# Performance work log

Measured on AMD Instinct MI355X. Metric: run time of the kernel, lower is better.

Reference implementation:

```python
import jax, jax.numpy as jnp
import numpy as np

B, NQ, NK = 1, 2048, 2048
A_DIM = M_DIM = 1024
H, KD, VD = 16, 64, 64


def setup_inputs() -> dict:
    key = jax.random.key(0)
    ks = jax.random.split(key, 8)
    return {
        "q_data": jax.random.normal(ks[0], (B, NQ, A_DIM), jnp.float32),
        "m_data": jax.random.normal(ks[1], (B, NK, M_DIM), jnp.float32),
        "batched_bias": jax.random.normal(ks[2], (B, H, NQ, NK), jnp.float32),
        "query_w": jax.random.normal(ks[3], (A_DIM, H, KD), jnp.float32) * 0.02,
        "query_b": jax.random.normal(ks[4], (1, H, KD), jnp.float32) * 0.02,
        "key_w": jax.random.normal(ks[5], (M_DIM, H, KD), jnp.float32) * 0.02,
        "value_w": jax.random.normal(ks[6], (M_DIM, H, VD), jnp.float32) * 0.02,
        "gating_w": jax.random.normal(ks[7], (A_DIM, H, VD), jnp.float32) * 0.02,
    }


def reference(q_data, m_data, batched_bias, query_w, query_b, key_w, value_w, gating_w):
    key_dim = query_w.shape[-1]
    scale = key_dim ** -0.5
    # fused: QKV projections + query bias + pair bias + softmax + gating
    q = (jnp.einsum('bqa,ahc->bqhc', q_data, query_w) + query_b) * scale  # [B,Q,H,KD]
    k = jnp.einsum('bka,ahc->bkhc', m_data, key_w)                        # [B,K,H,KD]
    v = jnp.einsum('bka,ahc->bkhc', m_data, value_w)                      # [B,K,H,VD]
    logits = jnp.einsum('bqhc,bkhc->bhqk', q, k) + batched_bias           # [B,H,Q,K]
    weights = jax.nn.softmax(logits, axis=-1)
    weighted = jnp.einsum('bhqk,bkhc->bqhc', weights, v)                  # [B,Q,H,VD]
    gate = jax.nn.sigmoid(jnp.einsum('bqa,ahc->bqhc', q_data, gating_w))  # [B,Q,H,VD]
    return gate * weighted
```

## Files before the change

kernel.cpp:

```cpp
#include <hip/hip_runtime.h>
#include <hip/hip_bf16.h>

typedef __bf16 bf16x8 __attribute__((ext_vector_type(8)));
typedef __bf16 bf16x4 __attribute__((ext_vector_type(4)));
typedef float  f32x4  __attribute__((ext_vector_type(4)));

typedef const __attribute__((address_space(1))) void* gptr_t;
typedef __attribute__((address_space(3))) void*       lptr_t;

#define NQ 2048
#define NK 2048
#define AD 1024
#define NH 16
#define HD 64
#define HC 1024

__global__ __launch_bounds__(256) void prep_convert(
    const float* __restrict__ q_data, const float* __restrict__ m_data,
    __bf16* __restrict__ aq, __bf16* __restrict__ am) {
  const int NEL4 = NQ * AD / 4;
  int gid = blockIdx.x * 256 + threadIdx.x;
  float4 v;
  __bf16* dst;
  if (gid < NEL4) { v = ((const float4*)q_data)[gid]; dst = aq + (size_t)gid * 4; }
  else            { v = ((const float4*)m_data)[gid - NEL4]; dst = am + (size_t)(gid - NEL4) * 4; }
  bf16x4 o;
  o[0] = (__bf16)v.x; o[1] = (__bf16)v.y; o[2] = (__bf16)v.z; o[3] = (__bf16)v.w;
  *(bf16x4*)dst = o;
}

__global__ __launch_bounds__(256) void prep_transpose(
    const float* __restrict__ w0, const float* __restrict__ w1,
    const float* __restrict__ w2, const float* __restrict__ w3,
    __bf16* __restrict__ t0, __bf16* __restrict__ t1,
    __bf16* __restrict__ t2, __bf16* __restrict__ t3) {
  __shared__ float tile[64][65];
  int b = blockIdx.x;
  int wsel = b >> 8;
  int t = b & 255;
  int a0 = (t >> 4) * 64, n0 = (t & 15) * 64;
  const float* W = (wsel == 0) ? w0 : (wsel == 1) ? w1 : (wsel == 2) ? w2 : w3;
  __bf16*      T = (wsel == 0) ? t0 : (wsel == 1) ? t1 : (wsel == 2) ? t2 : t3;
  int tx = threadIdx.x & 63, ty = threadIdx.x >> 6;
#pragma unroll
  for (int r = 0; r < 64; r += 4)
    tile[ty + r][tx] = W[(size_t)(a0 + ty + r) * HC + n0 + tx];
  __syncthreads();
#pragma unroll
  for (int r = 0; r < 64; r += 4)
    T[(size_t)(n0 + ty + r) * AD + a0 + tx] = (__bf16)tile[tx][ty + r];
}

__global__ __launch_bounds__(256) void proj_gemm(
    const __bf16* __restrict__ Aq, const __bf16* __restrict__ Am,
    const __bf16* __restrict__ Wq, const __bf16* __restrict__ Wk,
    const __bf16* __restrict__ Wv, const __bf16* __restrict__ Wg,
    const float* __restrict__ qbias,
    __bf16* __restrict__ qbf, __bf16* __restrict__ kb,
    __bf16* __restrict__ vt, float* __restrict__ gate) {
  __shared__ __bf16 As[128 * 32];
  __shared__ __bf16 Bs[128 * 32];
  int bx = blockIdx.x;
  int mode = bx >> 7, t = bx & 127;
  const __bf16 *A, *B;
  int bm, bn;
  if (mode == 2) {
    A = Wv; B = Am; bm = (t >> 4) << 7; bn = (t & 15) << 7;
  } else {
    bm = (t >> 3) << 7; bn = (t & 7) << 7;
    A = (mode == 1) ? Am : Aq;
    B = (mode == 0) ? Wq : (mode == 1) ? Wk : Wg;
  }
  int lane = threadIdx.x & 63, wave = threadIdx.x >> 6;
  int quad = lane >> 4, l15 = lane & 15;
  int wm = (wave >> 1) << 6, wn = (wave & 1) << 6;
  int srow = lane >> 2, schunk = lane & 3;

  f32x4 acc[4][4] = {};

  for (int k0 = 0; k0 < AD; k0 += 32) {
#pragma unroll
    for (int i = 0; i < 2; i++) {
      int inst = wave * 2 + i;
      int row = inst * 16 + srow;
      __builtin_amdgcn_global_load_lds(
          (gptr_t)((const char*)A + ((size_t)(bm + row) * AD + k0) * 2 + schunk * 16),
          (lptr_t)(As + inst * 512), 16, 0, 0);
      __builtin_amdgcn_global_load_lds(
          (gptr_t)((const char*)B + ((size_t)(bn + row) * AD + k0) * 2 + schunk * 16),
          (lptr_t)(Bs + inst * 512), 16, 0, 0);
    }
    __syncthreads();
    bf16x8 af[4], bfr[4];
#pragma unroll
    for (int i = 0; i < 4; i++) af[i]  = *(const bf16x8*)(As + (wm + i * 16 + l15) * 32 + quad * 8);
#pragma unroll
    for (int j = 0; j < 4; j++) bfr[j] = *(const bf16x8*)(Bs + (wn + j * 16 + l15) * 32 + quad * 8);
#pragma unroll
    for (int i = 0; i < 4; i++)
#pragma unroll
      for (int j = 0; j < 4; j++)
        acc[i][j] = __builtin_amdgcn_mfma_f32_16x16x32_bf16(af[i], bfr[j], acc[i][j], 0, 0, 0);
    __syncthreads();
  }

#pragma unroll
  for (int j = 0; j < 4; j++) {
    int n = bn + wn + j * 16 + l15;
    float qbb = (mode == 0) ? qbias[n] : 0.f;
#pragma unroll
    for (int i = 0; i < 4; i++) {
#pragma unroll
      for (int r = 0; r < 4; r++) {
        int m = bm + wm + i * 16 + quad * 4 + r;
        float v = acc[i][j][r];
        if (mode == 0) {
          int h = n >> 6, c = n & 63;
          qbf[((size_t)h * NQ + m) * HD + c] = (__bf16)((v + qbb) * 0.125f);
        } else if (mode == 1) {
          int h = n >> 6, c = n & 63;
          kb[((size_t)h * NK + m) * HD + c] = (__bf16)v;
        } else if (mode == 2) {
          vt[(size_t)m * NK + n] = (__bf16)v;
        } else {
          gate[(size_t)m * HC + n] = 1.f / (1.f + __expf(-v));
        }
      }
    }
  }
}

__global__ __launch_bounds__(256, 2) void attn(
    const __bf16* __restrict__ qbuf, const __bf16* __restrict__ kbuf,
    const __bf16* __restrict__ vtb, const float* __restrict__ gate,
    const float* __restrict__ bias, float* __restrict__ out) {
  __shared__ __bf16 Kt[2][64 * 64];
  __shared__ __bf16 Vt[2][64 * 64];
  __shared__ __bf16 P_lds[4][16 * 68];

  int bx = blockIdx.x;
  int h = bx & 15, qb0 = bx >> 4;
  int lane = threadIdx.x & 63, wave = threadIdx.x >> 6;
  int quad = lane >> 4, l15 = lane & 15;
  int qrow = (qb0 << 6) + wave * 16;

  const __bf16* qh = qbuf + (size_t)h * NQ * HD;
  const char*   kh = (const char*)(kbuf + (size_t)h * NK * HD);
  const char*   vh = (const char*)(vtb + (size_t)h * HD * NK);
  const float*  bh = bias + (size_t)h * NQ * NK;

  int srow = lane >> 3;
  int schunk = (lane & 7) ^ srow;

  bf16x8 a_q[2];
#pragma unroll
  for (int kk = 0; kk < 2; kk++)
    a_q[kk] = *(const bf16x8*)(qh + (size_t)(qrow + l15) * HD + quad * 8 + kk * 32);

  float lpart[4] = {0.f, 0.f, 0.f, 0.f};
  f32x4 acc_o[4] = {};
  __bf16* pl = &P_lds[wave][0];

#pragma unroll
  for (int j = 0; j < 2; j++) {
    int i = wave * 2 + j;
    __builtin_amdgcn_global_load_lds(
        (gptr_t)(kh + (size_t)(i * 8 + srow) * 128 + schunk * 16),
        (lptr_t)(&Kt[0][i * 512]), 16, 0, 0);
    __builtin_amdgcn_global_load_lds(
        (gptr_t)(vh + (size_t)(i * 8 + srow) * 4096 + schunk * 16),
        (lptr_t)(&Vt[0][i * 512]), 16, 0, 0);
  }

  f32x4 sp[4];
#pragma unroll
  for (int jt = 0; jt < 4; jt++)
#pragma unroll
    for (int r = 0; r < 4; r++)
      sp[jt][r] = bh[(size_t)(qrow + quad * 4 + r) * NK + jt * 16 + l15];

  for (int t = 0; t < 32; ++t) {
    int buf = t & 1;
    __syncthreads();

    if (t < 31) {
#pragma unroll
      for (int j = 0; j < 2; j++) {
        int i = wave * 2 + j;
        __builtin_amdgcn_global_load_lds(
            (gptr_t)(kh + (size_t)(t + 1) * 8192 + (size_t)(i * 8 + srow) * 128 + schunk * 16),
            (lptr_t)(&Kt[buf ^ 1][i * 512]), 16, 0, 0);
        __builtin_amdgcn_global_load_lds(
            (gptr_t)(vh + (size_t)(i * 8 + srow) * 4096 + (size_t)(t + 1) * 128 + schunk * 16),
            (lptr_t)(&Vt[buf ^ 1][i * 512]), 16, 0, 0);
      }
    }

    bf16x8 b_k[4][2], b_v[4][2];
#pragma unroll
    for (int jt = 0; jt < 4; jt++)
#pragma unroll
      for (int kk = 0; kk < 2; kk++) {
        int R = jt * 16 + l15;
        int pc = ((quad + 4 * kk) ^ (l15 & 7)) * 8;
        b_k[jt][kk] = *(const bf16x8*)(&Kt[buf][R * 64 + pc]);
        b_v[jt][kk] = *(const bf16x8*)(&Vt[buf][R * 64 + pc]);
      }

    f32x4 s[4];
#pragma unroll
    for (int jt = 0; jt < 4; jt++) s[jt] = sp[jt];

    if (t < 31) {
      const float* bn_ = bh + (t + 1) * 64;
#pragma unroll
      for (int jt = 0; jt < 4; jt++)
#pragma unroll
        for (int r = 0; r < 4; r++)
          sp[jt][r] = bn_[(size_t)(qrow + quad * 4 + r) * NK + jt * 16 + l15];
    }

#pragma unroll
    for (int jt = 0; jt < 4; jt++)
#pragma unroll
      for (int kk = 0; kk < 2; kk++)
        s[jt] = __builtin_amdgcn_mfma_f32_16x16x32_bf16(a_q[kk], b_k[jt][kk], s[jt], 0, 0, 0);

#pragma unroll
    for (int jt = 0; jt < 4; jt++)
#pragma unroll
      for (int r = 0; r < 4; r++) {
        float pv = __expf(s[jt][r]);
        lpart[r] += pv;
        pl[(quad * 4 + r) * 68 + jt * 16 + l15] = (__bf16)pv;
      }

    bf16x8 a_p[2];
#pragma unroll
    for (int kk = 0; kk < 2; kk++) {
      const __bf16* src = pl + l15 * 68 + quad * 8 + kk * 32;
      bf16x4 lo = *(const bf16x4*)src;
      bf16x4 hi = *(const bf16x4*)(src + 4);
      bf16x8 a;
#pragma unroll
      for (int j = 0; j < 4; j++) { a[j] = lo[j]; a[4 + j] = hi[j]; }
      a_p[kk] = a;
    }

#pragma unroll
    for (int jt = 0; jt < 4; jt++)
#pragma unroll
      for (int kk = 0; kk < 2; kk++)
        acc_o[jt] = __builtin_amdgcn_mfma_f32_16x16x32_bf16(a_p[kk], b_v[jt][kk], acc_o[jt], 0, 0, 0);
  }

#pragma unroll
  for (int off = 1; off < 16; off <<= 1)
#pragma unroll
    for (int r = 0; r < 4; r++) lpart[r] += __shfl_xor(lpart[r], off);
  float inv[4];
#pragma unroll
  for (int r = 0; r < 4; r++) inv[r] = 1.f / lpart[r];
#pragma unroll
  for (int jt = 0; jt < 4; jt++)
#pragma unroll
    for (int r = 0; r < 4; r++) {
      int q = qrow + quad * 4 + r;
      int d = jt * 16 + l15;
      float g = gate[(size_t)q * HC + h * HD + d];
      out[((size_t)q * NH + h) * HD + d] = acc_o[jt][r] * inv[r] * g;
    }
}

extern "C" void kernel_launch(void* const* d_in, const int* in_sizes, int n_in,
                              void* d_out, int out_size, void* d_ws, size_t ws_size,
                              hipStream_t stream) {
  const float* q_data   = (const float*)d_in[0];
  const float* m_data   = (const float*)d_in[1];
  const float* bias     = (const float*)d_in[2];
  const float* query_w  = (const float*)d_in[3];
  const float* query_b  = (const float*)d_in[4];
  const float* key_w    = (const float*)d_in[5];
  const float* value_w  = (const float*)d_in[6];
  const float* gating_w = (const float*)d_in[7];
  float* out = (float*)d_out;

  char* ws = (char*)d_ws;
  __bf16* Aq   = (__bf16*)(ws);
  __bf16* Am   = (__bf16*)(ws + ((size_t)4 << 20));
  __bf16* Wq   = (__bf16*)(ws + ((size_t)8 << 20));
  __bf16* Wk   = (__bf16*)(ws + ((size_t)10 << 20));
  __bf16* Wv   = (__bf16*)(ws + ((size_t)12 << 20));
  __bf16* Wg   = (__bf16*)(ws + ((size_t)14 << 20));
  __bf16* qbuf = (__bf16*)(ws + ((size_t)16 << 20));
  __bf16* kbuf = (__bf16*)(ws + ((size_t)20 << 20));
  __bf16* vtb  = (__bf16*)(ws + ((size_t)24 << 20));
  float*  gbuf = (float*)(ws + ((size_t)28 << 20));

  prep_convert<<<4096, 256, 0, stream>>>(q_data, m_data, Aq, Am);
  prep_transpose<<<1024, 256, 0, stream>>>(query_w, key_w, value_w, gating_w, Wq, Wk, Wv, Wg);
  proj_gemm<<<512, 256, 0, stream>>>(Aq, Am, Wq, Wk, Wv, Wg, query_b, qbuf, kbuf, vtb, gbuf);
  attn<<<512, 256, 0, stream>>>(qbuf, kbuf, vtb, gbuf, bias, out);
}
```

Baseline: 452.9 us.

## Widen attention K/V tile to 128 keys with vectorized bias loads

Each loop iteration now stages 128 keys of K and V into LDS instead of 64, halving the number of iterations and the barriers between them. The bias is read as float4 vectors by permuting the key-to-column mapping, so each lane owns four consecutive keys and writes P as bf16x4. The XOR swizzles are reworked for the wider tiles. In exchange the kernel uses twice the LDS for K/V, which may reduce occupancy, and it holds more bias prefetch registers.

```diff
diff --git a/kernel.cpp b/kernel.cpp
--- a/kernel.cpp
+++ b/kernel.cpp
@@ -134,8 +134,8 @@
     const __bf16* __restrict__ qbuf, const __bf16* __restrict__ kbuf,
     const __bf16* __restrict__ vtb, const float* __restrict__ gate,
     const float* __restrict__ bias, float* __restrict__ out) {
-  __shared__ __bf16 Kt[2][64 * 64];
-  __shared__ __bf16 Vt[2][64 * 64];
+  __shared__ __bf16 Kt[2][128 * 64];
+  __shared__ __bf16 Vt[2][64 * 128];
   __shared__ __bf16 P_lds[4][16 * 68];
 
   int bx = blockIdx.x;
@@ -145,12 +145,9 @@
   int qrow = (qb0 << 6) + wave * 16;
 
   const __bf16* qh = qbuf + (size_t)h * NQ * HD;
-  const char*   kh = (const char*)(kbuf + (size_t)h * NK * HD);
-  const char*   vh = (const char*)(vtb + (size_t)h * HD * NK);
+  const __bf16* kh = kbuf + (size_t)h * NK * HD;
+  const __bf16* vh = vtb + (size_t)h * HD * NK;
   const float*  bh = bias + (size_t)h * NQ * NK;
-
-  int srow = lane >> 3;
-  int schunk = (lane & 7) ^ srow;
 
   bf16x8 a_q[2];
 #pragma unroll
@@ -161,97 +158,120 @@
   f32x4 acc_o[4] = {};
   __bf16* pl = &P_lds[wave][0];
 
-#pragma unroll
-  for (int j = 0; j < 2; j++) {
-    int i = wave * 2 + j;
-    __builtin_amdgcn_global_load_lds(
-        (gptr_t)(kh + (size_t)(i * 8 + srow) * 128 + schunk * 16),
-        (lptr_t)(&Kt[0][i * 512]), 16, 0, 0);
-    __builtin_amdgcn_global_load_lds(
-        (gptr_t)(vh + (size_t)(i * 8 + srow) * 4096 + schunk * 16),
-        (lptr_t)(&Vt[0][i * 512]), 16, 0, 0);
-  }
-
-  f32x4 sp[4];
-#pragma unroll
-  for (int jt = 0; jt < 4; jt++)
+  int srowK = lane >> 3;
+  int srowV = lane >> 4;
+#define STAGE(bufi, k0s)                                                      \
+  {                                                                           \
+    _Pragma("unroll")                                                         \
+    for (int j = 0; j < 4; j++) {                                             \
+      int i = wave * 4 + j;                                                   \
+      int rK = i * 8 + srowK;                                                 \
+      int cK = (lane & 7) ^ ((2 * i + (srowK >> 2)) & 7);                     \
+      __builtin_amdgcn_global_load_lds(                                       \
+          (gptr_t)(kh + (size_t)(k0s + rK) * 64 + cK * 8),                    \
+          (lptr_t)(&Kt[bufi][i * 512]), 16, 0, 0);                            \
+      int rV = i * 4 + srowV;                                                 \
+      int cV = (lane & 15) ^ ((i * 4 + srowV) & 15);                          \
+      __builtin_amdgcn_global_load_lds(                                       \
+          (gptr_t)(vh + (size_t)rV * NK + k0s + cV * 8),                      \
+          (lptr_t)(&Vt[bufi][i * 512]), 16, 0, 0);                            \
+    }                                                                         \
+  }
+
+  STAGE(0, 0)
+
+  f32x4 spc[8];
+#pragma unroll
+  for (int s = 0; s < 2; s++)
 #pragma unroll
     for (int r = 0; r < 4; r++)
-      sp[jt][r] = bh[(size_t)(qrow + quad * 4 + r) * NK + jt * 16 + l15];
-
-  for (int t = 0; t < 32; ++t) {
+      spc[s * 4 + r] = *(const f32x4*)(bh + (size_t)(qrow + quad * 4 + r) * NK + s * 64 + 4 * l15);
+
+  for (int t = 0; t < 16; ++t) {
     int buf = t & 1;
     __syncthreads();
 
-    if (t < 31) {
-#pragma unroll
-      for (int j = 0; j < 2; j++) {
-        int i = wave * 2 + j;
-        __builtin_amdgcn_global_load_lds(
-            (gptr_t)(kh + (size_t)(t + 1) * 8192 + (size_t)(i * 8 + srow) * 128 + schunk * 16),
-            (lptr_t)(&Kt[buf ^ 1][i * 512]), 16, 0, 0);
-        __builtin_amdgcn_global_load_lds(
-            (gptr_t)(vh + (size_t)(i * 8 + srow) * 4096 + (size_t)(t + 1) * 128 + schunk * 16),
-            (lptr_t)(&Vt[buf ^ 1][i * 512]), 16, 0, 0);
+    if (t < 15) STAGE(buf ^ 1, (t + 1) * 128)
+
+    f32x4 s2[2][4];
+#pragma unroll
+    for (int s = 0; s < 2; s++)
+#pragma unroll
+      for (int jt = 0; jt < 4; jt++)
+#pragma unroll
+        for (int r = 0; r < 4; r++)
+          s2[s][jt][r] = spc[s * 4 + r][jt];
+
+    if (t < 15) {
+      const float* bn_ = bh + (size_t)(t + 1) * 128;
+#pragma unroll
+      for (int s = 0; s < 2; s++)
+#pragma unroll
+        for (int r = 0; r < 4; r++)
+          spc[s * 4 + r] = *(const f32x4*)(bn_ + (size_t)(qrow + quad * 4 + r) * NK + s * 64 + 4 * l15);
+    }
+
+    const __bf16* Kb = &Kt[buf][0];
+    const __bf16* Vb = &Vt[buf][0];
+
+#pragma unroll
+    for (int s = 0; s < 2; s++) {
+      bf16x8 b_k[4][2];
+#pragma unroll
+      for (int jt = 0; jt < 4; jt++)
+#pragma unroll
+        for (int kk = 0; kk < 2; kk++) {
+          int R = s * 64 + 4 * l15 + jt;
+          int pc = (quad + 4 * kk) ^ (l15 & 7);
+          b_k[jt][kk] = *(const bf16x8*)(Kb + R * 64 + pc * 8);
+        }
+
+#pragma unroll
+      for (int jt = 0; jt < 4; jt++)
+#pragma unroll
+        for (int kk = 0; kk < 2; kk++)
+          s2[s][jt] = __builtin_amdgcn_mfma_f32_16x16x32_bf16(a_q[kk], b_k[jt][kk], s2[s][jt], 0, 0, 0);
+
+#pragma unroll
+      for (int r = 0; r < 4; r++) {
+        bf16x4 w;
+#pragma unroll
+        for (int jt = 0; jt < 4; jt++) {
+          float pv = __expf(s2[s][jt][r]);
+          lpart[r] += pv;
+          w[jt] = (__bf16)pv;
+        }
+        *(bf16x4*)(pl + (quad * 4 + r) * 68 + 4 * l15) = w;
       }
-    }
-
-    bf16x8 b_k[4][2], b_v[4][2];
-#pragma unroll
-    for (int jt = 0; jt < 4; jt++)
+
+      bf16x8 a_p[2];
 #pragma unroll
       for (int kk = 0; kk < 2; kk++) {
-        int R = jt * 16 + l15;
-        int pc = ((quad + 4 * kk) ^ (l15 & 7)) * 8;
-        b_k[jt][kk] = *(const bf16x8*)(&Kt[buf][R * 64 + pc]);
-        b_v[jt][kk] = *(const bf16x8*)(&Vt[buf][R * 64 + pc]);
+        const __bf16* src = pl + l15 * 68 + quad * 8 + kk * 32;
+        bf16x4 lo = *(const bf16x4*)src;
+        bf16x4 hi = *(const bf16x4*)(src + 4);
+        bf16x8 a;
+#pragma unroll
+        for (int j = 0; j < 4; j++) { a[j] = lo[j]; a[4 + j] = hi[j]; }
+        a_p[kk] = a;
       }
 
-    f32x4 s[4];
-#pragma unroll
-    for (int jt = 0; jt < 4; jt++) s[jt] = sp[jt];
-
-    if (t < 31) {
-      const float* bn_ = bh + (t + 1) * 64;
-#pragma unroll
-      for (int jt = 0; jt < 4; jt++)
-#pragma unroll
-        for (int r = 0; r < 4; r++)
-          sp[jt][r] = bn_[(size_t)(qrow + quad * 4 + r) * NK + jt * 16 + l15];
-    }
-
-#pragma unroll
-    for (int jt = 0; jt < 4; jt++)
-#pragma unroll
-      for (int kk = 0; kk < 2; kk++)
-        s[jt] = __builtin_amdgcn_mfma_f32_16x16x32_bf16(a_q[kk], b_k[jt][kk], s[jt], 0, 0, 0);
-
-#pragma unroll
-    for (int jt = 0; jt < 4; jt++)
-#pragma unroll
-      for (int r = 0; r < 4; r++) {
-        float pv = __expf(s[jt][r]);
-        lpart[r] += pv;
-        pl[(quad * 4 + r) * 68 + jt * 16 + l15] = (__bf16)pv;
-      }
-
-    bf16x8 a_p[2];
-#pragma unroll
-    for (int kk = 0; kk < 2; kk++) {
-      const __bf16* src = pl + l15 * 68 + quad * 8 + kk * 32;
-      bf16x4 lo = *(const bf16x4*)src;
-      bf16x4 hi = *(const bf16x4*)(src + 4);
-      bf16x8 a;
-#pragma unroll
-      for (int j = 0; j < 4; j++) { a[j] = lo[j]; a[4 + j] = hi[j]; }
-      a_p[kk] = a;
-    }
-
-#pragma unroll
-    for (int jt = 0; jt < 4; jt++)
-#pragma unroll
-      for (int kk = 0; kk < 2; kk++)
-        acc_o[jt] = __builtin_amdgcn_mfma_f32_16x16x32_bf16(a_p[kk], b_v[jt][kk], acc_o[jt], 0, 0, 0);
+      bf16x8 b_v[4][2];
+#pragma unroll
+      for (int jt = 0; jt < 4; jt++)
+#pragma unroll
+        for (int kk = 0; kk < 2; kk++) {
+          int R = jt * 16 + l15;
+          int pc = (s * 8 + kk * 4 + quad) ^ l15;
+          b_v[jt][kk] = *(const bf16x8*)(Vb + R * 128 + pc * 8);
+        }
+
+#pragma unroll
+      for (int jt = 0; jt < 4; jt++)
+#pragma unroll
+        for (int kk = 0; kk < 2; kk++)
+          acc_o[jt] = __builtin_amdgcn_mfma_f32_16x16x32_bf16(a_p[kk], b_v[jt][kk], acc_o[jt], 0, 0, 0);
+    }
   }
 
 #pragma unroll
```

After: 438.7 us. 3.1% less time.
